# Optimization experiments

Hardware: AMD Instinct MI355X
Metric: run time of the kernel (lower is better)

The kernel has to match this reference:

```python
import jax, jax.numpy as jnp
import numpy as np

N, E, EL = 100000, 1600000, 200000
IN_FEATS, H, N_LAYERS = 128, 128, 3
HL = ((N_LAYERS + 1) * H) // 2  # PyG JK-LSTM hidden = (num_layers*channels)//2 = 256
EPS = 1e-5


def setup_inputs() -> dict:
    key = jax.random.key(0)
    ks = jax.random.split(key, 16)
    p = lambda k, shape: (jax.random.normal(k, shape, jnp.float32) * 0.05)
    return {
        "edge_index": jax.random.randint(ks[0], (2, E), 0, N),
        "x": jax.random.normal(ks[1], (N, IN_FEATS), jnp.float32),
        "edge_label_index": jax.random.randint(ks[2], (2, EL), 0, N),
        # GCNConv
        "gcn_w": p(ks[3], (IN_FEATS, H)), "gcn_b": jnp.zeros((H,), jnp.float32),
        # SGConv stack (lin applied AFTER propagation, K=1)
        "sg_w": p(ks[4], (N_LAYERS, H, H)), "sg_b": jnp.zeros((N_LAYERS, H), jnp.float32),
        # shared BatchNorm used between conv layers
        "bn_gamma": jnp.ones((H,), jnp.float32), "bn_beta": jnp.zeros((H,), jnp.float32),
        # bidirectional LSTM for JumpingKnowledge (torch gate order i,f,g,o)
        "w_ih_f": p(ks[5], (4 * HL, H)), "w_hh_f": p(ks[6], (4 * HL, HL)),
        "b_ih_f": jnp.zeros((4 * HL,), jnp.float32), "b_hh_f": jnp.zeros((4 * HL,), jnp.float32),
        "w_ih_b": p(ks[7], (4 * HL, H)), "w_hh_b": p(ks[8], (4 * HL, HL)),
        "b_ih_b": jnp.zeros((4 * HL,), jnp.float32), "b_hh_b": jnp.zeros((4 * HL,), jnp.float32),
        "att_w": p(ks[9], (2 * HL, 1)), "att_b": jnp.zeros((1,), jnp.float32),
        # edge predictor MLP
        "pred1_w": p(ks[10], (2 * H, H)), "pred1_b": jnp.zeros((H,), jnp.float32),
        "pbn_gamma": jnp.ones((H,), jnp.float32), "pbn_beta": jnp.zeros((H,), jnp.float32),
        "pred2_w": p(ks[11], (H, 1)), "pred2_b": jnp.zeros((1,), jnp.float32),
    }


def gcn_prop(x, src, dst, n):
    deg = jnp.zeros((n,), x.dtype).at[dst].add(jnp.ones((src.shape[0],), x.dtype)) + 1.0
    dinv = jax.lax.rsqrt(deg)
    norm = dinv[src] * dinv[dst]  # [E]
    out = jnp.zeros_like(x).at[dst].add(norm[:, None] * x[src])
    return out + (dinv * dinv)[:, None] * x  # self-loop contribution


def batchnorm(h, g, b):
    mu = h.mean(axis=0)
    var = ((h - mu) ** 2).mean(axis=0)
    return (h - mu) * jax.lax.rsqrt(var + EPS) * g + b


def lstm_dir(xs, w_ih, w_hh, b_ih, b_hh):
    # xs: [L, N, C] -> hidden states [L, N, HL]
    n = xs.shape[1]
    hh = w_hh.shape[1]
    def step(carry, xt):
        h, c = carry
        gates = xt @ w_ih.T + h @ w_hh.T + b_ih + b_hh
        i, f, g, o = jnp.split(gates, 4, axis=-1)
        c = jax.nn.sigmoid(f) * c + jax.nn.sigmoid(i) * jnp.tanh(g)
        h = jax.nn.sigmoid(o) * jnp.tanh(c)
        return (h, c), h
    init = (jnp.zeros((n, hh), xs.dtype), jnp.zeros((n, hh), xs.dtype))
    _, hs = jax.lax.scan(step, init, xs)
    return hs


def reference(edge_index, x, edge_label_index, gcn_w, gcn_b, sg_w, sg_b,
              bn_gamma, bn_beta, w_ih_f, w_hh_f, b_ih_f, b_hh_f,
              w_ih_b, w_hh_b, b_ih_b, b_hh_b, att_w, att_b,
              pred1_w, pred1_b, pbn_gamma, pbn_beta, pred2_w, pred2_b):
    src, dst = edge_index[0], edge_index[1]
    n = x.shape[0]
    hs = []
    # GCNConv: linear transform, then normalized propagation, then bias
    h = gcn_prop(x @ gcn_w, src, dst, n) + gcn_b
    h = batchnorm(jax.nn.relu(h), bn_gamma, bn_beta)  # dropout = identity (eval)
    hs.append(h)
    # SGConv (K=1): propagate then linear; last layer has no act/norm
    for i in range(N_LAYERS):
        h = gcn_prop(h, src, dst, n) @ sg_w[i] + sg_b[i]
        if i < N_LAYERS - 1:
            h = batchnorm(jax.nn.relu(h), bn_gamma, bn_beta)
        hs.append(h)
    xs = jnp.stack(hs, axis=0)  # [L, N, H]
    hf = lstm_dir(xs, w_ih_f, w_hh_f, b_ih_f, b_hh_f)
    hb = lstm_dir(xs[::-1], w_ih_b, w_hh_b, b_ih_b, b_hh_b)[::-1]
    seq = jnp.concatenate([hf, hb], axis=-1)  # [L, N, 2*HL]
    alpha = jax.nn.softmax((seq @ att_w)[..., 0] + att_b[0], axis=0)  # softmax over layers
    jk = jnp.einsum('lnh,ln->nh', xs, alpha)  # [N, H]
    # edge-level predictor
    row, col = edge_label_index[0], edge_label_index[1]
    z = jnp.concatenate([jk[row], jk[col]], axis=-1)  # [EL, 2H]
    z = jax.nn.relu(z @ pred1_w + pred1_b)
    z = batchnorm(z, pbn_gamma, pbn_beta)  # dropout = identity (eval)
    z = z @ pred2_w + pred2_b
    return jax.nn.sigmoid(z)
```

## Files before the change

### kernel.cpp

```cpp
#include <hip/hip_runtime.h>
#include <cstdint>

#define CDIV(a,b) (((a)+(b)-1)/(b))

typedef __bf16 bf16x8 __attribute__((ext_vector_type(8)));
typedef float  f32x4  __attribute__((ext_vector_type(4)));

__device__ __forceinline__ float bf2f(unsigned short u) {
    unsigned v = ((unsigned)u) << 16;
    float f; __builtin_memcpy(&f, &v, 4); return f;
}
__device__ __forceinline__ unsigned short f2bf(float f) {
    unsigned u; __builtin_memcpy(&u, &f, 4);
    u += 0x7fffu + ((u >> 16) & 1u);
    return (unsigned short)(u >> 16);
}
__device__ __forceinline__ float fsig(float x) { return 1.f / (1.f + __expf(-x)); }
__device__ __forceinline__ float ftanh(float x) { return 2.f * fsig(2.f * x) - 1.f; }

__device__ __forceinline__ void gld_lds16(const void* g, void* l) {
    __builtin_amdgcn_global_load_lds((__attribute__((address_space(1))) void*)(g),
                                     (__attribute__((address_space(3))) void*)(l), 16, 0, 0);
}


__global__ __launch_bounds__(256) void k_zero4(uint4* p, size_t n4) {
    size_t i = (size_t)blockIdx.x * 256 + threadIdx.x;
    if (i < n4) p[i] = make_uint4(0, 0, 0, 0);
}

__global__ __launch_bounds__(256) void k_deg(const int* ei, int* degi, int E) {
    int e = blockIdx.x * 256 + threadIdx.x;
    if (e < E) atomicAdd(&degi[ei[E + e]], 1);
}

__global__ __launch_bounds__(256) void k_dinv(const int* degi, float* dinv, int N) {
    int n = blockIdx.x * 256 + threadIdx.x;
    if (n < N) dinv[n] = rsqrtf((float)degi[n] + 1.f);
}

#define SCAN_B 2048
__global__ __launch_bounds__(256) void k_scan1(const int* in, int* out, int* bsum, int n) {
    __shared__ int ls[256];
    int b = blockIdx.x, t = threadIdx.x;
    int base = b * SCAN_B + t * 8;
    int v[8]; int s = 0;
#pragma unroll
    for (int i = 0; i < 8; ++i) { int idx = base + i; v[i] = (idx < n) ? in[idx] : 0; s += v[i]; }
    ls[t] = s; __syncthreads();
    for (int off = 1; off < 256; off <<= 1) {
        int x = (t >= off) ? ls[t - off] : 0;
        __syncthreads();
        ls[t] += x;
        __syncthreads();
    }
    int ex = ls[t] - s;
    if (t == 255) bsum[b] = ls[255];
    int run = ex;
#pragma unroll
    for (int i = 0; i < 8; ++i) { int idx = base + i; if (idx < n) out[idx] = run; run += v[i]; }
}
__global__ void k_scan2(int* bsum, int nb) {
    if (threadIdx.x == 0) {
        int acc = 0;
        for (int b = 0; b < nb; ++b) { int v = bsum[b]; bsum[b] = acc; acc += v; }
    }
}
__global__ __launch_bounds__(256) void k_scan3(int* rowp, int* curs, const int* bsum, int n) {
    int i = blockIdx.x * 256 + threadIdx.x;
    if (i < n) { int v = rowp[i] + bsum[i / SCAN_B]; rowp[i] = v; curs[i] = v; }
}
__global__ __launch_bounds__(256) void k_fill(const int* ei, int* curs, int* csr, int E) {
    int e = blockIdx.x * 256 + threadIdx.x;
    if (e < E) { int d = ei[E + e]; int pos = atomicAdd(&curs[d], 1); csr[pos] = ei[e]; }
}

__global__ __launch_bounds__(256) void k_xconv(const float* x, unsigned short* xb, int N, int Npad) {
    int idx = blockIdx.x * 256 + threadIdx.x;
    if (idx >= Npad * 64) return;
    int n = idx >> 6, q = idx & 63;
    ushort2 o;
    if (n < N) {
        float2 v = *(const float2*)&x[(size_t)n * 128 + q * 2];
        o = make_ushort2(f2bf(v.x), f2bf(v.y));
    } else o = make_ushort2(0, 0);
    *(ushort2*)&xb[(size_t)n * 128 + q * 2] = o;
}

__global__ __launch_bounds__(256) void k_packT(const float* W, unsigned short* BT, int K, int Nout) {
    int idx = blockIdx.x * 256 + threadIdx.x;
    if (idx >= K * Nout) return;
    int o = idx / K, k = idx % K;
    BT[idx] = f2bf(W[(size_t)k * Nout + o]);
}

__global__ __launch_bounds__(256) void k_packlstm4(const float* wih, const float* whh, unsigned short* BT) {
    int idx = blockIdx.x * 256 + threadIdx.x;
    if (idx >= 1024 * 384) return;
    int e = idx & 7, u = idx >> 3;
    int l4 = u & 3, l15 = (u >> 2) & 15, ni = (u >> 6) & 1;
    int rest = u >> 7;
    int ks = rest % 12, G = rest / 12;
    int gate = ni * 2 + (l15 >> 3);
    int hid = G * 8 + (l15 & 7);
    int srow = gate * 256 + hid;
    int k = ks * 32 + l4 * 8 + e;
    float v = (k < 128) ? wih[(size_t)srow * 128 + k] : whh[(size_t)srow * 256 + (k - 128)];
    BT[idx] = f2bf(v);
}
__global__ __launch_bounds__(256) void k_packbias4(const float* bih, const float* bhh, float* bias) {
    int c = blockIdx.x * 256 + threadIdx.x;
    if (c >= 1024) return;
    int G = c >> 5, cc = c & 31;
    int ni = cc >> 4, ll = cc & 15;
    int gate = ni * 2 + (ll >> 3);
    int hid = G * 8 + (ll & 7);
    int srow = gate * 256 + hid;
    bias[c] = bih[srow] + bhh[srow];
}


__global__ __launch_bounds__(256) void k_prop(const unsigned short* __restrict__ X,
                                              const int* __restrict__ rowp, const int* __restrict__ cnt,
                                              const int* __restrict__ csr, const float* __restrict__ dinv,
                                              const float* __restrict__ bias, int relu,
                                              int N, int Npad, unsigned short* __restrict__ OUT) {
    int node = (blockIdx.x * 256 + threadIdx.x) >> 4;
    if (node >= Npad) return;
    const int g = threadIdx.x & 15;
    unsigned short* op = OUT + (size_t)node * 128 + g * 8;
    if (node >= N) { *(uint4*)op = make_uint4(0, 0, 0, 0); return; }
    const int beg = rowp[node], num = cnt[node];
    const float di = dinv[node];
    float a[8];
#pragma unroll
    for (int j = 0; j < 8; ++j) a[j] = 0.f;
    for (int i = 0; i < num; ++i) {
        int s = csr[beg + i];
        float ws = dinv[s];
        uint4 q = *(const uint4*)&X[(size_t)s * 128 + g * 8];
        unsigned q0 = q.x, q1 = q.y, q2 = q.z, q3 = q.w;
        a[0] = fmaf(ws, bf2f((unsigned short)(q0 & 0xffffu)), a[0]);
        a[1] = fmaf(ws, bf2f((unsigned short)(q0 >> 16)), a[1]);
        a[2] = fmaf(ws, bf2f((unsigned short)(q1 & 0xffffu)), a[2]);
        a[3] = fmaf(ws, bf2f((unsigned short)(q1 >> 16)), a[3]);
        a[4] = fmaf(ws, bf2f((unsigned short)(q2 & 0xffffu)), a[4]);
        a[5] = fmaf(ws, bf2f((unsigned short)(q2 >> 16)), a[5]);
        a[6] = fmaf(ws, bf2f((unsigned short)(q3 & 0xffffu)), a[6]);
        a[7] = fmaf(ws, bf2f((unsigned short)(q3 >> 16)), a[7]);
    }
    uint4 xq = *(const uint4*)&X[(size_t)node * 128 + g * 8];
    unsigned x0 = xq.x, x1 = xq.y, x2 = xq.z, x3 = xq.w;
    const float dd = di * di;
    float o0 = di * a[0] + dd * bf2f((unsigned short)(x0 & 0xffffu));
    float o1 = di * a[1] + dd * bf2f((unsigned short)(x0 >> 16));
    float o2 = di * a[2] + dd * bf2f((unsigned short)(x1 & 0xffffu));
    float o3 = di * a[3] + dd * bf2f((unsigned short)(x1 >> 16));
    float o4 = di * a[4] + dd * bf2f((unsigned short)(x2 & 0xffffu));
    float o5 = di * a[5] + dd * bf2f((unsigned short)(x2 >> 16));
    float o6 = di * a[6] + dd * bf2f((unsigned short)(x3 & 0xffffu));
    float o7 = di * a[7] + dd * bf2f((unsigned short)(x3 >> 16));
    if (bias) {
        const float* bp = bias + g * 8;
        o0 += bp[0]; o1 += bp[1]; o2 += bp[2]; o3 += bp[3];
        o4 += bp[4]; o5 += bp[5]; o6 += bp[6]; o7 += bp[7];
    }
    if (relu) {
        o0 = fmaxf(o0, 0.f); o1 = fmaxf(o1, 0.f); o2 = fmaxf(o2, 0.f); o3 = fmaxf(o3, 0.f);
        o4 = fmaxf(o4, 0.f); o5 = fmaxf(o5, 0.f); o6 = fmaxf(o6, 0.f); o7 = fmaxf(o7, 0.f);
    }
    uint4 r;
    r.x = (unsigned)f2bf(o0) | ((unsigned)f2bf(o1) << 16);
    r.y = (unsigned)f2bf(o2) | ((unsigned)f2bf(o3) << 16);
    r.z = (unsigned)f2bf(o4) | ((unsigned)f2bf(o5) << 16);
    r.w = (unsigned)f2bf(o6) | ((unsigned)f2bf(o7) << 16);
    *(uint4*)op = r;
}


__global__ __launch_bounds__(256) void k_stats(const unsigned short* __restrict__ X, int rows, float* part) {
    __shared__ float ls[512];
    int t = threadIdx.x, b = blockIdx.x;
    int ch = t & 127, half = t >> 7;
    float s = 0.f, s2 = 0.f;
    for (int r = b * 2 + half; r < rows; r += 512) {
        float v = bf2f(X[(size_t)r * 128 + ch]);
        s += v; s2 += v * v;
    }
    ls[t] = s; ls[256 + t] = s2;
    __syncthreads();
    if (t < 128) {
        part[b * 256 + t] = ls[t] + ls[t + 128];
        part[b * 256 + 128 + t] = ls[256 + t] + ls[256 + t + 128];
    }
}
__global__ void k_bnfinal(const float* part, int nb, float rows,
                          const float* gamma, const float* beta, float* bnst) {
    int ch = threadIdx.x;
    if (ch >= 128) return;
    float s = 0.f, s2 = 0.f;
    for (int b = 0; b < nb; ++b) { s += part[b * 256 + ch]; s2 += part[b * 256 + 128 + ch]; }
    float mu = s / rows, var = s2 / rows - mu * mu;
    float sc = gamma[ch] * rsqrtf(var + 1e-5f);
    bnst[ch] = sc;
    bnst[128 + ch] = beta[ch] - mu * sc;
}
__global__ __launch_bounds__(256) void k_apply(const unsigned short* in, const float* bnst,
                                               unsigned short* outv, int N, int Npad) {
    int idx = blockIdx.x * 256 + threadIdx.x;
    if (idx >= Npad * 64) return;
    int n = idx >> 6, q = idx & 63;
    ushort2 o;
    if (n < N) {
        ushort2 v = *(const ushort2*)&in[(size_t)n * 128 + q * 2];
        int c0 = q * 2;
        o = make_ushort2(f2bf(bf2f(v.x) * bnst[c0] + bnst[128 + c0]),
                         f2bf(bf2f(v.y) * bnst[c0 + 1] + bnst[128 + c0 + 1]));
    } else o = make_ushort2(0, 0);
    *(ushort2*)&outv[(size_t)n * 128 + q * 2] = o;
}


template<int GATHER>
__device__ __forceinline__ void gemm_core(
    const unsigned short* __restrict__ A0, int lda0, int K0,
    const unsigned short* __restrict__ A1, int lda1, int Ktot,
    const unsigned short* __restrict__ BT, int ldb,
    const int* __restrict__ gR, const int* __restrict__ gC, int ELr,
    int m0, int c0, unsigned short* sA, unsigned short* sB, f32x4 acc[4][4]) {
    const int tid = threadIdx.x;
    const int wid = tid >> 6, lane = tid & 63;
    const int l15 = lane & 15, l4 = lane >> 4;
    const int wr = (wid >> 1) * 64, wc = (wid & 1) * 64;
    const int crow = lane >> 3;
    const int cslot = (lane & 7) ^ crow;
    const int nK = Ktot >> 6;
    for (int ks = 0; ks < nK; ++ks) {
        const int k0 = ks << 6;
#pragma unroll
        for (int i = 0; i < 4; ++i) {
            const int chunk = wid * 4 + i;
            const int row = chunk * 8 + crow;
            const unsigned short* bs = BT + (size_t)(c0 + row) * ldb + k0 + (cslot << 3);
            gld_lds16(bs, sB + chunk * 512);
            if constexpr (GATHER) {
                int e = m0 + row; if (e >= ELr) e = ELr - 1;
                const int nid = (k0 < K0) ? gR[e] : gC[e];
                const unsigned short* as = A0 + (size_t)nid * lda0 + (k0 & (K0 - 1)) + (lane & 7) * 8;
                *(uint4*)(sA + chunk * 512 + crow * 64 + (((lane & 7) ^ crow) << 3)) = *(const uint4*)as;
            } else {
                const unsigned short* as = (k0 < K0)
                    ? A0 + (size_t)(m0 + row) * lda0 + k0 + (cslot << 3)
                    : A1 + (size_t)(m0 + row) * lda1 + (k0 - K0) + (cslot << 3);
                gld_lds16(as, sA + chunk * 512);
            }
        }
        __syncthreads();
#pragma unroll
        for (int kk = 0; kk < 2; ++kk) {
            const int c8 = kk * 4 + l4;
            const int rs = l15 & 7;
            bf16x8 av[4], bv[4];
#pragma unroll
            for (int i = 0; i < 4; ++i)
                av[i] = *(const bf16x8*)(sA + (wr + i * 16 + l15) * 64 + ((c8 ^ rs) << 3));
#pragma unroll
            for (int i = 0; i < 4; ++i)
                bv[i] = *(const bf16x8*)(sB + (wc + i * 16 + l15) * 64 + ((c8 ^ rs) << 3));
#pragma unroll
            for (int mi = 0; mi < 4; ++mi)
#pragma unroll
                for (int ni = 0; ni < 4; ++ni)
                    acc[mi][ni] = __builtin_amdgcn_mfma_f32_16x16x32_bf16(av[mi], bv[ni], acc[mi][ni], 0, 0, 0);
        }
        __syncthreads();
    }
}

template<int GATHER>
__global__ __launch_bounds__(256) void k_gemm(
    const unsigned short* __restrict__ A0, int lda0, int K0,
    const unsigned short* __restrict__ A1, int lda1, int Ktot,
    const unsigned short* __restrict__ BT, int ldb,
    const int* __restrict__ gR, const int* __restrict__ gC, int ELr,
    const float* __restrict__ bias, int relu,
    unsigned short* __restrict__ C, int ldc, int NT) {
    extern __shared__ char smem[];
    unsigned short* sA = (unsigned short*)smem;
    unsigned short* sB = (unsigned short*)(smem + 16384);
    int mt = blockIdx.x / NT, nt = blockIdx.x % NT;
    int m0 = mt * 128, c0 = nt * 128;
    f32x4 acc[4][4];
#pragma unroll
    for (int a = 0; a < 4; ++a)
#pragma unroll
        for (int b = 0; b < 4; ++b) acc[a][b] = (f32x4){0.f, 0.f, 0.f, 0.f};
    gemm_core<GATHER>(A0, lda0, K0, A1, lda1, Ktot, BT, ldb, gR, gC, ELr, m0, c0, sA, sB, acc);
    const int tid = threadIdx.x;
    const int wid = tid >> 6, lane = tid & 63;
    const int l15 = lane & 15, l4 = lane >> 4;
    const int wr = (wid >> 1) * 64, wc = (wid & 1) * 64;
#pragma unroll
    for (int ni = 0; ni < 4; ++ni) {
        int col = c0 + wc + ni * 16 + l15;
        float bv = bias ? bias[col] : 0.f;
#pragma unroll
        for (int mi = 0; mi < 4; ++mi) {
            int rbase = m0 + wr + mi * 16 + l4 * 4;
#pragma unroll
            for (int j = 0; j < 4; ++j) {
                float v = acc[mi][ni][j] + bv;
                if (relu) v = fmaxf(v, 0.f);
                C[(size_t)(rbase + j) * ldc + col] = f2bf(v);
            }
        }
    }
}


__global__ __launch_bounds__(512)
void k_lstm_fused(
    const unsigned short* __restrict__ xs,
    const unsigned short* __restrict__ BT2f, const unsigned short* __restrict__ BT2b,
    const float* __restrict__ bias2f, const float* __restrict__ bias2b,
    const float* __restrict__ att_w,
    float* __restrict__ scores,
    int N, int Npad) {
    __shared__ unsigned short xls[64 * 128];
    __shared__ unsigned short hbuf[2][64 * 256];
    __shared__ float c_ld[64 * 256];
    __shared__ float sc_ld[8][64];

    const int tid = threadIdx.x;
    const int wid = tid >> 6, lane = tid & 63;
    const int l15 = lane & 15, l4 = lane >> 4;
    const int rs = l15 & 7;
    const int m0 = blockIdx.x * 64;
    const int loff = (l15 * 4 + l4) * 8;
    const bool hi = (l15 & 8) != 0;

    float scl[4] = {0.f, 0.f, 0.f, 0.f};

#pragma unroll 1
    for (int dir = 0; dir < 2; ++dir) {
        const unsigned short* BT2 = dir ? BT2b : BT2f;
        const float* bias2 = dir ? bias2b : bias2f;
        const float* attw = att_w + dir * 256;
        for (int i = tid; i < 2048; i += 512) ((uint4*)hbuf[0])[i] = make_uint4(0, 0, 0, 0);
        for (int i = tid; i < 4096; i += 512) ((uint4*)c_ld)[i] = make_uint4(0, 0, 0, 0);
        __syncthreads();
        unsigned short* hcur = hbuf[0];
        unsigned short* hnxt = hbuf[1];

#pragma unroll 1
        for (int t = 0; t < 4; ++t) {
            const int lyr = dir ? (3 - t) : t;
            {
                const unsigned short* xl = xs + (size_t)lyr * Npad * 128;
#pragma unroll
                for (int i = 0; i < 2; ++i) {
                    int chunk = wid * 2 + i;
                    int row = chunk * 4 + l4;
                    gld_lds16(xl + (size_t)(m0 + row) * 128 + ((l15 ^ (row & 7)) << 3),
                              xls + chunk * 512);
                }
            }
            __syncthreads();

            float scA[4], scB[4];
#pragma unroll
            for (int a = 0; a < 4; ++a) { scA[a] = 0.f; scB[a] = 0.f; }

#pragma unroll 1
            for (int p = 0; p < 4; ++p) {
                const int G = wid * 4 + p;
                f32x4 acc[4][2];
#pragma unroll
                for (int a = 0; a < 4; ++a) {
                    acc[a][0] = (f32x4){0.f, 0.f, 0.f, 0.f};
                    acc[a][1] = (f32x4){0.f, 0.f, 0.f, 0.f};
                }
                const unsigned short* bp = BT2 + (size_t)G * 12288 + loff;
                bf16x8 f0a = *(const bf16x8*)(bp);
                bf16x8 f0b = *(const bf16x8*)(bp + 512);
                bf16x8 f1a = *(const bf16x8*)(bp + 1024);
                bf16x8 f1b = *(const bf16x8*)(bp + 1536);
#pragma unroll 1
                for (int ks = 0; ks < 4; ++ks) {
                    bf16x8 bv0 = f0a, bv1 = f0b;
                    f0a = f1a; f0b = f1b;
                    f1a = *(const bf16x8*)(bp + ((ks + 2) * 2 + 0) * 512);
                    f1b = *(const bf16x8*)(bp + ((ks + 2) * 2 + 1) * 512);
#pragma unroll
                    for (int mi = 0; mi < 4; ++mi) {
                        bf16x8 av = *(const bf16x8*)(xls + (mi * 16 + l15) * 128 +
                                                     (((ks * 4 + l4) ^ rs) << 3));
                        acc[mi][0] = __builtin_amdgcn_mfma_f32_16x16x32_bf16(av, bv0, acc[mi][0], 0, 0, 0);
                        acc[mi][1] = __builtin_amdgcn_mfma_f32_16x16x32_bf16(av, bv1, acc[mi][1], 0, 0, 0);
                    }
                }
#pragma unroll 1
                for (int ks = 4; ks < 12; ++ks) {
                    bf16x8 bv0 = f0a, bv1 = f0b;
                    f0a = f1a; f0b = f1b;
                    f1a = *(const bf16x8*)(bp + ((ks + 2) * 2 + 0) * 512);
                    f1b = *(const bf16x8*)(bp + ((ks + 2) * 2 + 1) * 512);
#pragma unroll
                    for (int mi = 0; mi < 4; ++mi) {
                        bf16x8 av = *(const bf16x8*)(hcur + (mi * 16 + l15) * 256 +
                                                     ((((ks - 4) * 4 + l4) ^ rs) << 3));
                        acc[mi][0] = __builtin_amdgcn_mfma_f32_16x16x32_bf16(av, bv0, acc[mi][0], 0, 0, 0);
                        acc[mi][1] = __builtin_amdgcn_mfma_f32_16x16x32_bf16(av, bv1, acc[mi][1], 0, 0, 0);
                    }
                }
                const float bi0 = bias2[G * 32 + l15];
                const float bi1 = bias2[G * 32 + 16 + l15];
                const float aw = attw[G * 8 + (l15 & 7)];
#pragma unroll
                for (int mi = 0; mi < 4; ++mi) {
                    float a00 = acc[mi][0][0] + bi0, a01 = acc[mi][0][1] + bi0;
                    float a02 = acc[mi][0][2] + bi0, a03 = acc[mi][0][3] + bi0;
                    float a10 = acc[mi][1][0] + bi1, a11 = acc[mi][1][1] + bi1;
                    float a12 = acc[mi][1][2] + bi1, a13 = acc[mi][1][3] + bi1;
                    float r0 = __shfl_xor(hi ? a00 : a02, 8);
                    float r1 = __shfl_xor(hi ? a01 : a03, 8);
                    float r2 = __shfl_xor(hi ? a10 : a12, 8);
                    float r3 = __shfl_xor(hi ? a11 : a13, 8);
                    float iA = hi ? r0  : a00,  fA = hi ? a02 : r0;
                    float gA = hi ? r2  : a10,  oA = hi ? a12 : r2;
                    float iB = hi ? r1  : a01,  fB = hi ? a03 : r1;
                    float gB = hi ? r3  : a11,  oB = hi ? a13 : r3;
                    const int rA = mi * 16 + l4 * 4 + (hi ? 2 : 0);
                    {
                        float gi = fsig(iA), gf = fsig(fA), gg = ftanh(gA), go = fsig(oA);
                        const int ca = rA * 256 + (((G ^ ((rA >> 2) & 7)) << 3) + (l15 & 7));
                        float cc = fmaf(gf, c_ld[ca], gi * gg);
                        c_ld[ca] = cc;
                        float hn = go * ftanh(cc);
                        scA[mi] = fmaf(hn, aw, scA[mi]);
                        *(unsigned short*)((char*)hnxt + rA * 512 +
                                           ((G ^ (rA & 7)) << 4) + (l15 & 7) * 2) = f2bf(hn);
                    }
                    {
                        const int rB = rA + 1;
                        float gi = fsig(iB), gf = fsig(fB), gg = ftanh(gB), go = fsig(oB);
                        const int cb = rB * 256 + (((G ^ ((rB >> 2) & 7)) << 3) + (l15 & 7));
                        float cc = fmaf(gf, c_ld[cb], gi * gg);
                        c_ld[cb] = cc;
                        float hn = go * ftanh(cc);
                        scB[mi] = fmaf(hn, aw, scB[mi]);
                        *(unsigned short*)((char*)hnxt + rB * 512 +
                                           ((G ^ (rB & 7)) << 4) + (l15 & 7) * 2) = f2bf(hn);
                    }
                }
            }
#pragma unroll
            for (int mi = 0; mi < 4; ++mi) {
                float sA = scA[mi], sB = scB[mi];
                sA += __shfl_xor(sA, 1); sA += __shfl_xor(sA, 2); sA += __shfl_xor(sA, 4);
                sB += __shfl_xor(sB, 1); sB += __shfl_xor(sB, 2); sB += __shfl_xor(sB, 4);
                if ((l15 & 7) == 0) {
                    int row = mi * 16 + l4 * 4 + (hi ? 2 : 0);
                    sc_ld[wid][row] = sA;
                    sc_ld[wid][row + 1] = sB;
                }
            }
            __syncthreads();
            if (tid < 64) {
                float s = 0.f;
#pragma unroll
                for (int w = 0; w < 8; ++w) s += sc_ld[w][tid];
#pragma unroll
                for (int l = 0; l < 4; ++l) scl[l] += (l == lyr) ? s : 0.f;
            }
            unsigned short* tmp = hcur; hcur = hnxt; hnxt = tmp;
        }
    }
    if (tid < 64) {
        int n = m0 + tid;
        if (n < N) {
#pragma unroll
            for (int l = 0; l < 4; ++l) scores[(size_t)l * N + n] = scl[l];
        }
    }
}


__global__ __launch_bounds__(256) void k_jk(const float* __restrict__ sc, const unsigned short* __restrict__ xs,
                                            unsigned short* __restrict__ jk, int N, int Npad) {
    int gw = (blockIdx.x * 256 + threadIdx.x) >> 6;
    if (gw >= N) return;
    int lane = threadIdx.x & 63;
    float s0 = sc[gw], s1 = sc[N + gw], s2 = sc[2 * N + gw], s3 = sc[3 * N + gw];
    float m = fmaxf(fmaxf(s0, s1), fmaxf(s2, s3));
    float e0 = __expf(s0 - m), e1 = __expf(s1 - m), e2 = __expf(s2 - m), e3 = __expf(s3 - m);
    float inv = 1.f / (e0 + e1 + e2 + e3);
    float a0 = e0 * inv, a1 = e1 * inv, a2 = e2 * inv, a3 = e3 * inv;
    size_t stride = (size_t)Npad * 128;
    const unsigned short* p = xs + (size_t)gw * 128 + lane * 2;
    ushort2 v0 = *(const ushort2*)p;
    ushort2 v1 = *(const ushort2*)(p + stride);
    ushort2 v2 = *(const ushort2*)(p + 2 * stride);
    ushort2 v3 = *(const ushort2*)(p + 3 * stride);
    float r0 = a0 * bf2f(v0.x) + a1 * bf2f(v1.x) + a2 * bf2f(v2.x) + a3 * bf2f(v3.x);
    float r1 = a0 * bf2f(v0.y) + a1 * bf2f(v1.y) + a2 * bf2f(v2.y) + a3 * bf2f(v3.y);
    *(ushort2*)&jk[(size_t)gw * 128 + lane * 2] = make_ushort2(f2bf(r0), f2bf(r1));
}

__global__ __launch_bounds__(256) void k_final(const unsigned short* __restrict__ z1, const float* __restrict__ bnst,
                                               const float* __restrict__ w2, const float* __restrict__ b2,
                                               float* __restrict__ out, int EL) {
    int e = (blockIdx.x * 256 + threadIdx.x) >> 6;
    if (e >= EL) return;
    int lane = threadIdx.x & 63;
    ushort2 z = *(const ushort2*)&z1[(size_t)e * 128 + lane * 2];
    int c0 = lane * 2;
    float y0 = bf2f(z.x) * bnst[c0] + bnst[128 + c0];
    float y1 = bf2f(z.y) * bnst[c0 + 1] + bnst[128 + c0 + 1];
    float p = y0 * w2[c0] + y1 * w2[c0 + 1];
#pragma unroll
    for (int off = 32; off; off >>= 1) p += __shfl_xor(p, off);
    if (lane == 0) out[e] = 1.f / (1.f + __expf(-(p + b2[0])));
}


extern "C" void kernel_launch(void* const* d_in, const int* in_sizes, int n_in,
                              void* d_out, int out_size, void* d_ws, size_t ws_size,
                              hipStream_t stream) {
    const int* ei      = (const int*)d_in[0];
    const float* x     = (const float*)d_in[1];
    const int* eli     = (const int*)d_in[2];
    const float* gcn_w = (const float*)d_in[3];
    const float* gcn_b = (const float*)d_in[4];
    const float* sg_w  = (const float*)d_in[5];
    const float* sg_b  = (const float*)d_in[6];
    const float* bn_g  = (const float*)d_in[7];
    const float* bn_b  = (const float*)d_in[8];
    const float* w_ih_f = (const float*)d_in[9];
    const float* w_hh_f = (const float*)d_in[10];
    const float* b_ih_f = (const float*)d_in[11];
    const float* b_hh_f = (const float*)d_in[12];
    const float* w_ih_b = (const float*)d_in[13];
    const float* w_hh_b = (const float*)d_in[14];
    const float* b_ih_b = (const float*)d_in[15];
    const float* b_hh_b = (const float*)d_in[16];
    const float* att_w = (const float*)d_in[17];
    const float* p1_w  = (const float*)d_in[19];
    const float* p1_b  = (const float*)d_in[20];
    const float* pbn_g = (const float*)d_in[21];
    const float* pbn_b = (const float*)d_in[22];
    const float* p2_w  = (const float*)d_in[23];
    const float* p2_b  = (const float*)d_in[24];

    const int E = in_sizes[0] / 2;
    const int N = in_sizes[1] / 128;
    const int EL = in_sizes[2] / 2;
    const int Npad = CDIV(N, 128) * 128;
    const int ELpad = CDIV(EL, 128) * 128;
    const size_t NB128 = (size_t)Npad * 128 * 2;

    char* wsp = (char*)d_ws;
    size_t off = 0;
    auto A = [&](size_t b) -> char* {
        char* p = wsp + off;
        off = (off + b + 255) & ~(size_t)255;
        return p;
    };
    int* degi = (int*)A((size_t)N * 4);
    float* dinv = (float*)A((size_t)N * 4);
    int* rowp = (int*)A((size_t)N * 4);
    int* curs = (int*)A((size_t)N * 4);
    int* bsum = (int*)A(256 * 4);
    unsigned short* gT   = (unsigned short*)A(128 * 128 * 2);
    unsigned short* sgT  = (unsigned short*)A(3 * 128 * 128 * 2);
    unsigned short* p1T  = (unsigned short*)A(128 * 256 * 2);
    unsigned short* BTf  = (unsigned short*)A(1024 * 384 * 2);
    unsigned short* BTb  = (unsigned short*)A(1024 * 384 * 2);
    float* biasf = (float*)A(1024 * 4);
    float* biasb = (float*)A(1024 * 4);
    float* part = (float*)A(256 * 256 * 4);
    float* bnst = (float*)A(256 * 4);
    float* scores = (float*)A((size_t)4 * N * 4);
    unsigned short* xs = (unsigned short*)A(NB128 * 4);
    const size_t arena0 = off;
    int* csr = (int*)A((size_t)E * 4);
    unsigned short* xb   = (unsigned short*)A(NB128);
    unsigned short* bufA = (unsigned short*)A(NB128);
    unsigned short* bufB = (unsigned short*)A(NB128);
    const size_t convEnd = off;
    off = arena0;
    unsigned short* jk = (unsigned short*)A((size_t)N * 128 * 2);
    unsigned short* z1 = (unsigned short*)A((size_t)ELpad * 128 * 2);
    const size_t predEnd = off;
    if (convEnd > ws_size || predEnd > ws_size) return;

    k_zero4<<<CDIV((size_t)N * 4, 16 * 256), 256, 0, stream>>>((uint4*)degi, CDIV((size_t)N * 4, 16));
    k_deg<<<CDIV(E, 256), 256, 0, stream>>>(ei, degi, E);
    k_dinv<<<CDIV(N, 256), 256, 0, stream>>>(degi, dinv, N);
    int nb = CDIV(N, SCAN_B);
    k_scan1<<<nb, 256, 0, stream>>>(degi, rowp, bsum, N);
    k_scan2<<<1, 64, 0, stream>>>(bsum, nb);
    k_scan3<<<CDIV(N, 256), 256, 0, stream>>>(rowp, curs, bsum, N);
    k_fill<<<CDIV(E, 256), 256, 0, stream>>>(ei, curs, csr, E);

    k_xconv<<<CDIV(Npad * 64, 256), 256, 0, stream>>>(x, xb, N, Npad);
    k_packT<<<CDIV(128 * 128, 256), 256, 0, stream>>>(gcn_w, gT, 128, 128);
    for (int i = 0; i < 3; ++i)
        k_packT<<<CDIV(128 * 128, 256), 256, 0, stream>>>(sg_w + (size_t)i * 128 * 128, sgT + (size_t)i * 128 * 128, 128, 128);
    k_packT<<<CDIV(256 * 128, 256), 256, 0, stream>>>(p1_w, p1T, 256, 128);
    k_packlstm4<<<CDIV(1024 * 384, 256), 256, 0, stream>>>(w_ih_f, w_hh_f, BTf);
    k_packlstm4<<<CDIV(1024 * 384, 256), 256, 0, stream>>>(w_ih_b, w_hh_b, BTb);
    k_packbias4<<<4, 256, 0, stream>>>(b_ih_f, b_hh_f, biasf);
    k_packbias4<<<4, 256, 0, stream>>>(b_ih_b, b_hh_b, biasb);

    const int MT = Npad / 128;
    k_gemm<0><<<MT, 256, 32768, stream>>>(xb, 128, 128, nullptr, 0, 128, gT, 128,
                                          nullptr, nullptr, 0, nullptr, 0, bufA, 128, 1);
    k_prop<<<CDIV(Npad * 16, 256), 256, 0, stream>>>(bufA, rowp, degi, csr, dinv, gcn_b, 1, N, Npad, bufB);
    k_stats<<<256, 256, 0, stream>>>(bufB, N, part);
    k_bnfinal<<<1, 128, 0, stream>>>(part, 256, (float)N, bn_g, bn_b, bnst);
    k_apply<<<CDIV(Npad * 64, 256), 256, 0, stream>>>(bufB, bnst, xs, N, Npad);

    for (int i = 0; i < 3; ++i) {
        k_prop<<<CDIV(Npad * 16, 256), 256, 0, stream>>>(xs + (size_t)i * Npad * 128, rowp, degi, csr, dinv,
                                                         nullptr, 0, N, Npad, bufA);
        unsigned short* dst = (i < 2) ? bufB : xs + (size_t)3 * Npad * 128;
        k_gemm<0><<<MT, 256, 32768, stream>>>(bufA, 128, 128, nullptr, 0, 128,
                                              sgT + (size_t)i * 128 * 128, 128,
                                              nullptr, nullptr, 0, sg_b + i * 128, (i < 2) ? 1 : 0, dst, 128, 1);
        if (i < 2) {
            k_stats<<<256, 256, 0, stream>>>(bufB, N, part);
            k_bnfinal<<<1, 128, 0, stream>>>(part, 256, (float)N, bn_g, bn_b, bnst);
            k_apply<<<CDIV(Npad * 64, 256), 256, 0, stream>>>(bufB, bnst, xs + (size_t)(i + 1) * Npad * 128, N, Npad);
        }
    }

    k_lstm_fused<<<Npad / 64, 512, 0, stream>>>(xs, BTf, BTb, biasf, biasb, att_w, scores, N, Npad);

    k_jk<<<CDIV(N * 64, 256), 256, 0, stream>>>(scores, xs, jk, N, Npad);

    const int MTe = ELpad / 128;
    k_gemm<1><<<MTe, 256, 32768, stream>>>(jk, 128, 128, nullptr, 0, 256, p1T, 256,
                                           eli, eli + EL, EL, p1_b, 1, z1, 128, 1);
    k_stats<<<256, 256, 0, stream>>>(z1, EL, part);
    k_bnfinal<<<1, 128, 0, stream>>>(part, 256, (float)EL, pbn_g, pbn_b, bnst);
    k_final<<<CDIV(EL * 64, 256), 256, 0, stream>>>(z1, bnst, p2_w, p2_b, (float*)d_out, EL);
    (void)n_in; (void)out_size;
}
```

Measured before the change: 2.613 ms.

## Keep LSTM cell state in registers, single h buffer, prefetch next neighbor in prop

```diff
diff --git a/kernel.cpp b/kernel.cpp
--- a/kernel.cpp
+++ b/kernel.cpp
@@ -135,19 +135,25 @@
     float a[8];
 #pragma unroll
     for (int j = 0; j < 8; ++j) a[j] = 0.f;
-    for (int i = 0; i < num; ++i) {
-        int s = csr[beg + i];
+    if (num > 0) {
+        int s = csr[beg];
         float ws = dinv[s];
         uint4 q = *(const uint4*)&X[(size_t)s * 128 + g * 8];
-        unsigned q0 = q.x, q1 = q.y, q2 = q.z, q3 = q.w;
-        a[0] = fmaf(ws, bf2f((unsigned short)(q0 & 0xffffu)), a[0]);
-        a[1] = fmaf(ws, bf2f((unsigned short)(q0 >> 16)), a[1]);
-        a[2] = fmaf(ws, bf2f((unsigned short)(q1 & 0xffffu)), a[2]);
-        a[3] = fmaf(ws, bf2f((unsigned short)(q1 >> 16)), a[3]);
-        a[4] = fmaf(ws, bf2f((unsigned short)(q2 & 0xffffu)), a[4]);
-        a[5] = fmaf(ws, bf2f((unsigned short)(q2 >> 16)), a[5]);
-        a[6] = fmaf(ws, bf2f((unsigned short)(q3 & 0xffffu)), a[6]);
-        a[7] = fmaf(ws, bf2f((unsigned short)(q3 >> 16)), a[7]);
+        for (int i = 0; i < num; ++i) {
+            int sn = (i + 1 < num) ? csr[beg + i + 1] : s;
+            float wn = dinv[sn];
+            uint4 qn = *(const uint4*)&X[(size_t)sn * 128 + g * 8];
+            unsigned q0 = q.x, q1 = q.y, q2 = q.z, q3 = q.w;
+            a[0] = fmaf(ws, bf2f((unsigned short)(q0 & 0xffffu)), a[0]);
+            a[1] = fmaf(ws, bf2f((unsigned short)(q0 >> 16)), a[1]);
+            a[2] = fmaf(ws, bf2f((unsigned short)(q1 & 0xffffu)), a[2]);
+            a[3] = fmaf(ws, bf2f((unsigned short)(q1 >> 16)), a[3]);
+            a[4] = fmaf(ws, bf2f((unsigned short)(q2 & 0xffffu)), a[4]);
+            a[5] = fmaf(ws, bf2f((unsigned short)(q2 >> 16)), a[5]);
+            a[6] = fmaf(ws, bf2f((unsigned short)(q3 & 0xffffu)), a[6]);
+            a[7] = fmaf(ws, bf2f((unsigned short)(q3 >> 16)), a[7]);
+            s = sn; ws = wn; q = qn;
+        }
     }
     uint4 xq = *(const uint4*)&X[(size_t)node * 128 + g * 8];
     unsigned x0 = xq.x, x1 = xq.y, x2 = xq.z, x3 = xq.w;
@@ -327,8 +333,7 @@
     float* __restrict__ scores,
     int N, int Npad) {
     __shared__ unsigned short xls[64 * 128];
-    __shared__ unsigned short hbuf[2][64 * 256];
-    __shared__ float c_ld[64 * 256];
+    __shared__ unsigned short hls[64 * 256];
     __shared__ float sc_ld[8][64];
 
     const int tid = threadIdx.x;
@@ -346,11 +351,14 @@
         const unsigned short* BT2 = dir ? BT2b : BT2f;
         const float* bias2 = dir ? bias2b : bias2f;
         const float* attw = att_w + dir * 256;
-        for (int i = tid; i < 2048; i += 512) ((uint4*)hbuf[0])[i] = make_uint4(0, 0, 0, 0);
-        for (int i = tid; i < 4096; i += 512) ((uint4*)c_ld)[i] = make_uint4(0, 0, 0, 0);
+        for (int i = tid; i < 2048; i += 512) ((uint4*)hls)[i] = make_uint4(0, 0, 0, 0);
         __syncthreads();
-        unsigned short* hcur = hbuf[0];
-        unsigned short* hnxt = hbuf[1];
+        float c0[4][2], c1[4][2], c2[4][2], c3[4][2];
+#pragma unroll
+        for (int a = 0; a < 4; ++a) {
+            c0[a][0] = 0.f; c0[a][1] = 0.f; c1[a][0] = 0.f; c1[a][1] = 0.f;
+            c2[a][0] = 0.f; c2[a][1] = 0.f; c3[a][0] = 0.f; c3[a][1] = 0.f;
+        }
 
 #pragma unroll 1
         for (int t = 0; t < 4; ++t) {
@@ -370,9 +378,9 @@
             float scA[4], scB[4];
 #pragma unroll
             for (int a = 0; a < 4; ++a) { scA[a] = 0.f; scB[a] = 0.f; }
-
-#pragma unroll 1
-            for (int p = 0; p < 4; ++p) {
+            unsigned hn_pk[16];
+
+            auto do_pass = [&](int p, float (&cp)[4][2], unsigned* hp) {
                 const int G = wid * 4 + p;
                 f32x4 acc[4][2];
 #pragma unroll
@@ -380,17 +388,11 @@
                     acc[a][0] = (f32x4){0.f, 0.f, 0.f, 0.f};
                     acc[a][1] = (f32x4){0.f, 0.f, 0.f, 0.f};
                 }
-                const unsigned short* bp = BT2 + (size_t)G * 12288 + loff;
-                bf16x8 f0a = *(const bf16x8*)(bp);
-                bf16x8 f0b = *(const bf16x8*)(bp + 512);
-                bf16x8 f1a = *(const bf16x8*)(bp + 1024);
-                bf16x8 f1b = *(const bf16x8*)(bp + 1536);
+                const unsigned short* bpp = BT2 + (size_t)G * 12288 + loff;
 #pragma unroll 1
                 for (int ks = 0; ks < 4; ++ks) {
-                    bf16x8 bv0 = f0a, bv1 = f0b;
-                    f0a = f1a; f0b = f1b;
-                    f1a = *(const bf16x8*)(bp + ((ks + 2) * 2 + 0) * 512);
-                    f1b = *(const bf16x8*)(bp + ((ks + 2) * 2 + 1) * 512);
+                    bf16x8 bv0 = *(const bf16x8*)(bpp + (ks * 2 + 0) * 512);
+                    bf16x8 bv1 = *(const bf16x8*)(bpp + (ks * 2 + 1) * 512);
 #pragma unroll
                     for (int mi = 0; mi < 4; ++mi) {
                         bf16x8 av = *(const bf16x8*)(xls + (mi * 16 + l15) * 128 +
@@ -401,13 +403,11 @@
                 }
 #pragma unroll 1
                 for (int ks = 4; ks < 12; ++ks) {
-                    bf16x8 bv0 = f0a, bv1 = f0b;
-                    f0a = f1a; f0b = f1b;
-                    f1a = *(const bf16x8*)(bp + ((ks + 2) * 2 + 0) * 512);
-                    f1b = *(const bf16x8*)(bp + ((ks + 2) * 2 + 1) * 512);
+                    bf16x8 bv0 = *(const bf16x8*)(bpp + (ks * 2 + 0) * 512);
+                    bf16x8 bv1 = *(const bf16x8*)(bpp + (ks * 2 + 1) * 512);
 #pragma unroll
                     for (int mi = 0; mi < 4; ++mi) {
-                        bf16x8 av = *(const bf16x8*)(hcur + (mi * 16 + l15) * 256 +
+                        bf16x8 av = *(const bf16x8*)(hls + (mi * 16 + l15) * 256 +
                                                      ((((ks - 4) * 4 + l4) ^ rs) << 3));
                         acc[mi][0] = __builtin_amdgcn_mfma_f32_16x16x32_bf16(av, bv0, acc[mi][0], 0, 0, 0);
                         acc[mi][1] = __builtin_amdgcn_mfma_f32_16x16x32_bf16(av, bv1, acc[mi][1], 0, 0, 0);
@@ -430,30 +430,31 @@
                     float gA = hi ? r2  : a10,  oA = hi ? a12 : r2;
                     float iB = hi ? r1  : a01,  fB = hi ? a03 : r1;
                     float gB = hi ? r3  : a11,  oB = hi ? a13 : r3;
-                    const int rA = mi * 16 + l4 * 4 + (hi ? 2 : 0);
+                    unsigned pk;
                     {
                         float gi = fsig(iA), gf = fsig(fA), gg = ftanh(gA), go = fsig(oA);
-                        const int ca = rA * 256 + (((G ^ ((rA >> 2) & 7)) << 3) + (l15 & 7));
-                        float cc = fmaf(gf, c_ld[ca], gi * gg);
-                        c_ld[ca] = cc;
+                        float cc = fmaf(gf, cp[mi][0], gi * gg);
+                        cp[mi][0] = cc;
                         float hn = go * ftanh(cc);
                         scA[mi] = fmaf(hn, aw, scA[mi]);
-                        *(unsigned short*)((char*)hnxt + rA * 512 +
-                                           ((G ^ (rA & 7)) << 4) + (l15 & 7) * 2) = f2bf(hn);
+                        pk = (unsigned)f2bf(hn);
                     }
                     {
-                        const int rB = rA + 1;
                         float gi = fsig(iB), gf = fsig(fB), gg = ftanh(gB), go = fsig(oB);
-                        const int cb = rB * 256 + (((G ^ ((rB >> 2) & 7)) << 3) + (l15 & 7));
-                        float cc = fmaf(gf, c_ld[cb], gi * gg);
-                        c_ld[cb] = cc;
+                        float cc = fmaf(gf, cp[mi][1], gi * gg);
+                        cp[mi][1] = cc;
                         float hn = go * ftanh(cc);
                         scB[mi] = fmaf(hn, aw, scB[mi]);
-                        *(unsigned short*)((char*)hnxt + rB * 512 +
-                                           ((G ^ (rB & 7)) << 4) + (l15 & 7) * 2) = f2bf(hn);
+                        pk |= ((unsigned)f2bf(hn)) << 16;
                     }
+                    hp[mi] = pk;
                 }
-            }
+            };
+            do_pass(0, c0, hn_pk + 0);
+            do_pass(1, c1, hn_pk + 4);
+            do_pass(2, c2, hn_pk + 8);
+            do_pass(3, c3, hn_pk + 12);
+
 #pragma unroll
             for (int mi = 0; mi < 4; ++mi) {
                 float sA = scA[mi], sB = scB[mi];
@@ -473,7 +474,23 @@
 #pragma unroll
                 for (int l = 0; l < 4; ++l) scl[l] += (l == lyr) ? s : 0.f;
             }
-            unsigned short* tmp = hcur; hcur = hnxt; hnxt = tmp;
+#pragma unroll
+            for (int p = 0; p < 4; ++p) {
+                const int G = wid * 4 + p;
+#pragma unroll
+                for (int mi = 0; mi < 4; ++mi) {
+                    unsigned v = hn_pk[p * 4 + mi];
+                    const int rA = mi * 16 + l4 * 4 + (hi ? 2 : 0);
+                    *(unsigned short*)((char*)hls + rA * 512 +
+                                       ((G ^ (rA & 7)) << 4) + (l15 & 7) * 2) =
+                        (unsigned short)(v & 0xffffu);
+                    const int rB = rA + 1;
+                    *(unsigned short*)((char*)hls + rB * 512 +
+                                       ((G ^ (rB & 7)) << 4) + (l15 & 7) * 2) =
+                        (unsigned short)(v >> 16);
+                }
+            }
+            __syncthreads();
         }
     }
     if (tid < 64) {
```

Result: slower. 3.435 ms (+31.5%).
